# Performance work log

Measured on AMD Instinct MI355X. Metric: run time of the kernel, lower is better.

Reference implementation:

```python
import jax, jax.numpy as jnp
import numpy as np

D_MODEL = 768
N_HEAD = 12
BATCH = 2
SEQ = 2048
MASK_FILL = -100000.0


def setup_inputs() -> dict:
    key = jax.random.key(0)
    ks = jax.random.split(key, 10)
    s = 1.0 / np.sqrt(D_MODEL)
    inp = {
        "xEnc": jax.random.normal(ks[0], (BATCH, SEQ, D_MODEL), jnp.float32),
        "xDec": jax.random.normal(ks[1], (BATCH, SEQ, D_MODEL), jnp.float32),
        # causal mask: True where attention is disallowed (j > i)
        "mask": (jnp.arange(SEQ)[None, :] > jnp.arange(SEQ)[:, None])[None, None, :, :],
        "wQ": jax.random.uniform(ks[2], (D_MODEL, D_MODEL), jnp.float32, -s, s),
        "bQ": jax.random.uniform(ks[3], (D_MODEL,), jnp.float32, -s, s),
        "wK": jax.random.uniform(ks[4], (D_MODEL, D_MODEL), jnp.float32, -s, s),
        "bK": jax.random.uniform(ks[5], (D_MODEL,), jnp.float32, -s, s),
        "wV": jax.random.uniform(ks[6], (D_MODEL, D_MODEL), jnp.float32, -s, s),
        "bV": jax.random.uniform(ks[7], (D_MODEL,), jnp.float32, -s, s),
        "wOut": jax.random.uniform(ks[8], (D_MODEL, D_MODEL), jnp.float32, -s, s),
        "bOut": jax.random.uniform(ks[9], (D_MODEL,), jnp.float32, -s, s),
    }
    return inp


def reference(xEnc, xDec, mask, wQ, bQ, wK, bK, wV, bV, wOut, bOut):
    B, S, D = xEnc.shape
    H = N_HEAD
    Dh = D // H
    # torch Linear: y = x @ W.T + b
    Q = xDec @ wQ.T + bQ
    K = xEnc @ wK.T + bK
    V = xEnc @ wV.T + bV
    Q = Q.reshape(B, S, H, Dh).transpose(0, 2, 1, 3)  # [B,H,S,Dh]
    K = K.reshape(B, S, H, Dh).transpose(0, 2, 1, 3)
    V = V.reshape(B, S, H, Dh).transpose(0, 2, 1, 3)
    score = jnp.einsum("bhqd,bhkd->bhqk", Q, K) / jnp.sqrt(jnp.float32(Dh))
    score = jnp.where(mask, MASK_FILL, score)
    attn = jax.nn.softmax(score, axis=-1)
    ctx = jnp.einsum("bhqk,bhkd->bhqd", attn, V)  # [B,H,S,Dh]
    ctx = ctx.transpose(0, 2, 1, 3).reshape(B, S, D)
    return ctx @ wOut.T + bOut
```

## Files before the change

kernel.cpp:

```cpp
#include <hip/hip_runtime.h>
#include <stdint.h>
#include <stddef.h>

#define DMODEL 768
#define NHEAD 12
#define SEQLEN 2048
#define NBATCH 2
#define DH 64
#define MTOT (NBATCH*SEQLEN)

typedef short s16x4 __attribute__((ext_vector_type(4)));
typedef short s16x8 __attribute__((ext_vector_type(8)));
typedef float f32x4 __attribute__((ext_vector_type(4)));

#define XDECB_OFF 0u
#define XENCB_OFF 3145728u
#define WQB_OFF   6291456u
#define WKB_OFF   6881280u
#define WVB_OFF   7471104u
#define WOUTB_OFF 8060928u
#define QB_OFF    8650752u
#define KB_OFF    11796480u
#define VT_OFF    14942208u
#define CTXB_OFF  18087936u

#define QSCALE 0.18033688011112042f

static __device__ __forceinline__ unsigned short f2bf(float f) {
  union { float f; unsigned int u; } v; v.f = f;
  unsigned int r = v.u + 0x7fffu + ((v.u >> 16) & 1u);
  return (unsigned short)(r >> 16);
}

static __device__ __forceinline__ unsigned int pack2bf(float f0, float f1) {
  union { float f; unsigned int u; } a, b; a.f = f0; b.f = f1;
  return __builtin_amdgcn_perm(b.u + 0x8000u, a.u + 0x8000u, 0x07060302u);
}

#if __has_builtin(__builtin_amdgcn_exp2f)
#define EXP2(x) __builtin_amdgcn_exp2f(x)
#else
#define EXP2(x) exp2f(x)
#endif

static __device__ __forceinline__ f32x4 mfma16(s16x4 a, s16x4 b, f32x4 c) {
  return __builtin_amdgcn_mfma_f32_16x16x16bf16_1k(a, b, c, 0, 0, 0);
}
static __device__ __forceinline__ f32x4 mfma32(s16x8 a, s16x8 b, f32x4 c) {
  return __builtin_amdgcn_mfma_f32_16x16x32_bf16(a, b, c, 0, 0, 0);
}

__global__ __launch_bounds__(256) void cvt_kernel(
    const float* __restrict__ xDec, const float* __restrict__ xEnc,
    const float* __restrict__ wQ, const float* __restrict__ wK,
    const float* __restrict__ wV, const float* __restrict__ wOut,
    unsigned short* __restrict__ ws)
{
  const int seg = blockIdx.y;
  const float* src;
  unsigned int n4, off;
  switch (seg) {
    case 0:  src = xDec; n4 = 786432; off = XDECB_OFF; break;
    case 1:  src = xEnc; n4 = 786432; off = XENCB_OFF; break;
    case 2:  src = wQ;   n4 = 147456; off = WQB_OFF;   break;
    case 3:  src = wK;   n4 = 147456; off = WKB_OFF;   break;
    case 4:  src = wV;   n4 = 147456; off = WVB_OFF;   break;
    default: src = wOut; n4 = 147456; off = WOUTB_OFF; break;
  }
  unsigned short* d = ws + off;
  const unsigned int stride = gridDim.x * blockDim.x;
  for (unsigned int i = blockIdx.x * blockDim.x + threadIdx.x; i < n4; i += stride) {
    const float4 v = ((const float4*)src)[i];
    s16x4 p;
    p[0] = (short)f2bf(v.x); p[1] = (short)f2bf(v.y);
    p[2] = (short)f2bf(v.z); p[3] = (short)f2bf(v.w);
    ((s16x4*)d)[i] = p;
  }
}

#define LSTR 72

__global__ __launch_bounds__(256, 4) void qkv_gemm(
    const unsigned short* __restrict__ xDecB, const unsigned short* __restrict__ xEncB,
    const unsigned short* __restrict__ wQB, const unsigned short* __restrict__ wKB,
    const unsigned short* __restrict__ wVB,
    const float* __restrict__ bQ, const float* __restrict__ bK, const float* __restrict__ bV,
    unsigned short* __restrict__ Qb, unsigned short* __restrict__ Kb,
    unsigned short* __restrict__ Vt)
{
  const int z = blockIdx.z;
  const unsigned short* __restrict__ A = (z == 0) ? xDecB : xEncB;
  const unsigned short* __restrict__ B = (z == 0) ? wQB : ((z == 1) ? wKB : wVB);
  const float* __restrict__ bias = (z == 0) ? bQ : ((z == 1) ? bK : bV);

  __shared__ unsigned short lA[64 * LSTR];
  __shared__ unsigned short lB[128 * LSTR];

  const int tid  = threadIdx.x;
  const int lane = tid & 63;
  const int wid  = tid >> 6;
  const int ln   = lane & 15;
  const int qd   = lane >> 4;
  const int m0 = blockIdx.x * 64;
  const int n0 = blockIdx.y * 128;
  const int wm = (wid & 1) * 32;
  const int wn = (wid >> 1) * 64;

  f32x4 acc[2][4] = {};
  s16x8 pA[2], pB[4];

  auto load_tile = [&](int k0) {
    #pragma unroll
    for (int i = 0; i < 2; ++i) {
      const int f = tid + i * 256;
      pA[i] = *(const s16x8*)(A + (size_t)(m0 + (f >> 3)) * DMODEL + k0 + (f & 7) * 8);
    }
    #pragma unroll
    for (int i = 0; i < 4; ++i) {
      const int f = tid + i * 256;
      pB[i] = *(const s16x8*)(B + (size_t)(n0 + (f >> 3)) * DMODEL + k0 + (f & 7) * 8);
    }
  };

  load_tile(0);
  for (int k0 = 0; k0 < DMODEL; k0 += 64) {
    #pragma unroll
    for (int i = 0; i < 2; ++i) {
      const int f = tid + i * 256;
      *(s16x8*)&lA[(f >> 3) * LSTR + (f & 7) * 8] = pA[i];
    }
    #pragma unroll
    for (int i = 0; i < 4; ++i) {
      const int f = tid + i * 256;
      *(s16x8*)&lB[(f >> 3) * LSTR + (f & 7) * 8] = pB[i];
    }
    __syncthreads();
    if (k0 + 64 < DMODEL) load_tile(k0 + 64);
    #pragma unroll
    for (int kc = 0; kc < 2; ++kc) {
      s16x8 af[2], bfr[4];
      #pragma unroll
      for (int i = 0; i < 2; ++i)
        af[i] = *(const s16x8*)&lA[(wm + i * 16 + ln) * LSTR + kc * 32 + qd * 8];
      #pragma unroll
      for (int j = 0; j < 4; ++j)
        bfr[j] = *(const s16x8*)&lB[(wn + j * 16 + ln) * LSTR + kc * 32 + qd * 8];
      #pragma unroll
      for (int i = 0; i < 2; ++i)
        #pragma unroll
        for (int j = 0; j < 4; ++j)
          acc[i][j] = mfma32(af[i], bfr[j], acc[i][j]);
    }
    __syncthreads();
  }

  #pragma unroll
  for (int j = 0; j < 4; ++j) {
    const int n_g = n0 + wn + j * 16 + ln;
    const float bv = bias[n_g];
    const int h    = n_g >> 6;
    const int dcol = n_g & 63;
    #pragma unroll
    for (int i = 0; i < 2; ++i) {
      #pragma unroll
      for (int r = 0; r < 4; ++r) {
        const int m_g  = m0 + wm + i * 16 + qd * 4 + r;
        const int bb   = m_g >> 11;
        const int srow = m_g & 2047;
        const float val = acc[i][j][r] + bv;
        if (z == 0)
          Qb[((size_t)((bb * NHEAD + h) * SEQLEN + srow)) * DH + dcol] = f2bf(val * QSCALE);
        else if (z == 1)
          Kb[((size_t)((bb * NHEAD + h) * SEQLEN + srow)) * DH + dcol] = f2bf(val);
        else
          Vt[((size_t)((bb * NHEAD + h) * DH + dcol)) * SEQLEN + srow] = f2bf(val);
      }
    }
  }
}

__global__ __launch_bounds__(256, 4) void out_gemm(
    const unsigned short* __restrict__ ctx, const unsigned short* __restrict__ wOutB,
    const float* __restrict__ bOut, float* __restrict__ out)
{
  __shared__ unsigned short lA[64 * LSTR];
  __shared__ unsigned short lB[128 * LSTR];

  const int tid  = threadIdx.x;
  const int lane = tid & 63;
  const int wid  = tid >> 6;
  const int ln   = lane & 15;
  const int qd   = lane >> 4;
  const int m0 = blockIdx.x * 64;
  const int n0 = blockIdx.y * 128;
  const int wm = (wid & 1) * 32;
  const int wn = (wid >> 1) * 64;

  f32x4 acc[2][4] = {};
  s16x8 pA[2], pB[4];

  auto load_tile = [&](int k0) {
    #pragma unroll
    for (int i = 0; i < 2; ++i) {
      const int f = tid + i * 256;
      pA[i] = *(const s16x8*)(ctx + (size_t)(m0 + (f >> 3)) * DMODEL + k0 + (f & 7) * 8);
    }
    #pragma unroll
    for (int i = 0; i < 4; ++i) {
      const int f = tid + i * 256;
      pB[i] = *(const s16x8*)(wOutB + (size_t)(n0 + (f >> 3)) * DMODEL + k0 + (f & 7) * 8);
    }
  };

  load_tile(0);
  for (int k0 = 0; k0 < DMODEL; k0 += 64) {
    #pragma unroll
    for (int i = 0; i < 2; ++i) {
      const int f = tid + i * 256;
      *(s16x8*)&lA[(f >> 3) * LSTR + (f & 7) * 8] = pA[i];
    }
    #pragma unroll
    for (int i = 0; i < 4; ++i) {
      const int f = tid + i * 256;
      *(s16x8*)&lB[(f >> 3) * LSTR + (f & 7) * 8] = pB[i];
    }
    __syncthreads();
    if (k0 + 64 < DMODEL) load_tile(k0 + 64);
    #pragma unroll
    for (int kc = 0; kc < 2; ++kc) {
      s16x8 af[2], bfr[4];
      #pragma unroll
      for (int i = 0; i < 2; ++i)
        af[i] = *(const s16x8*)&lA[(wm + i * 16 + ln) * LSTR + kc * 32 + qd * 8];
      #pragma unroll
      for (int j = 0; j < 4; ++j)
        bfr[j] = *(const s16x8*)&lB[(wn + j * 16 + ln) * LSTR + kc * 32 + qd * 8];
      #pragma unroll
      for (int i = 0; i < 2; ++i)
        #pragma unroll
        for (int j = 0; j < 4; ++j)
          acc[i][j] = mfma32(af[i], bfr[j], acc[i][j]);
    }
    __syncthreads();
  }

  #pragma unroll
  for (int j = 0; j < 4; ++j) {
    const int n_g = n0 + wn + j * 16 + ln;
    const float bv = bOut[n_g];
    #pragma unroll
    for (int i = 0; i < 2; ++i) {
      #pragma unroll
      for (int r = 0; r < 4; ++r) {
        const int m_g = m0 + wm + i * 16 + qd * 4 + r;
        out[(size_t)m_g * DMODEL + n_g] = acc[i][j][r] + bv;
      }
    }
  }
}

#define KVT 128
#define LKP 72
#define LVP 136

__global__ __launch_bounds__(256, 3) void attn_kernel(
    const unsigned short* __restrict__ Qb, const unsigned short* __restrict__ Kb,
    const unsigned short* __restrict__ Vt, unsigned short* __restrict__ ctx)
{
  __shared__ unsigned short lK[KVT * LKP];
  __shared__ unsigned short lV[DH * LVP];

  const int tid  = threadIdx.x;
  const int lane = tid & 63;
  const int wid  = tid >> 6;
  const int ln   = lane & 15;
  const int qd   = lane >> 4;
  const int bh = blockIdx.y;
  const int q0 = (gridDim.x - 1 - blockIdx.x) * 64;
  const int q_lane = q0 + wid * 16 + ln;

  s16x8 qf[2];
  {
    const unsigned short* Qrow = Qb + ((size_t)bh * SEQLEN + q_lane) * DH;
    qf[0] = *(const s16x8*)(Qrow + qd * 8);
    qf[1] = *(const s16x8*)(Qrow + 32 + qd * 8);
  }

  float m_run = -__builtin_inff();
  float l_run = 0.0f;
  f32x4 o_acc[4] = {};

  const unsigned short* Kbase = Kb + (size_t)bh * SEQLEN * DH;
  const unsigned short* Vbase = Vt + (size_t)bh * DH * SEQLEN;
  const int kv_end = q0 + 64;
  const int ntiles = (kv_end + KVT - 1) / KVT;

  s16x8 rK[4], rV[4];
  auto load_kv = [&](int kv0) {
    #pragma unroll
    for (int i = 0; i < 4; ++i) {
      const int f = tid + i * 256;
      rK[i] = *(const s16x8*)(Kbase + (size_t)(kv0 + (f >> 3)) * DH + (f & 7) * 8);
    }
    #pragma unroll
    for (int i = 0; i < 4; ++i) {
      const int f = tid + i * 256;
      rV[i] = *(const s16x8*)(Vbase + (size_t)(f >> 4) * SEQLEN + kv0 + (f & 15) * 8);
    }
  };

  load_kv(0);
  for (int t0 = 0; t0 < ntiles; ++t0) {
    const int kv0 = t0 * KVT;
    #pragma unroll
    for (int i = 0; i < 4; ++i) {
      const int f = tid + i * 256;
      *(s16x8*)&lK[(f >> 3) * LKP + (f & 7) * 8] = rK[i];
    }
    #pragma unroll
    for (int i = 0; i < 4; ++i) {
      const int f = tid + i * 256;
      *(s16x8*)&lV[(f >> 4) * LVP + (f & 15) * 8] = rV[i];
    }
    __syncthreads();
    if (t0 + 1 < ntiles) load_kv(kv0 + KVT);

    f32x4 s_acc[8] = {};
    #pragma unroll
    for (int kc = 0; kc < 2; ++kc) {
      #pragma unroll
      for (int t = 0; t < 8; ++t) {
        const s16x8 a = *(const s16x8*)&lK[(t * 16 + ln) * LKP + kc * 32 + qd * 8];
        s_acc[t] = mfma32(a, qf[kc], s_acc[t]);
      }
    }

    float tmax = -1e30f;
    if (kv0 + KVT > q0) {
      #pragma unroll
      for (int t = 0; t < 8; ++t) {
        #pragma unroll
        for (int r = 0; r < 4; ++r) {
          const int kv = kv0 + t * 16 + qd * 4 + r;
          float sv = s_acc[t][r];
          sv = (kv > q_lane) ? -1e30f : sv;
          s_acc[t][r] = sv;
          tmax = fmaxf(tmax, sv);
        }
      }
    } else {
      #pragma unroll
      for (int t = 0; t < 8; ++t) {
        #pragma unroll
        for (int r = 0; r < 4; ++r)
          tmax = fmaxf(tmax, s_acc[t][r]);
      }
    }
    tmax = fmaxf(tmax, __shfl_xor(tmax, 16));
    tmax = fmaxf(tmax, __shfl_xor(tmax, 32));
    const float m_new = fmaxf(m_run, tmax);
    const float alpha = EXP2(m_run - m_new);

    float rsum = 0.0f;
    s16x4 pf[8];
    #pragma unroll
    for (int t = 0; t < 8; ++t) {
      const float p0 = EXP2(s_acc[t][0] - m_new);
      const float p1 = EXP2(s_acc[t][1] - m_new);
      const float p2 = EXP2(s_acc[t][2] - m_new);
      const float p3 = EXP2(s_acc[t][3] - m_new);
      rsum += (p0 + p1) + (p2 + p3);
      union { unsigned int u[2]; s16x4 v; } pk;
      pk.u[0] = pack2bf(p0, p1);
      pk.u[1] = pack2bf(p2, p3);
      pf[t] = pk.v;
    }
    rsum += __shfl_xor(rsum, 16);
    rsum += __shfl_xor(rsum, 32);
    l_run = l_run * alpha + rsum;
    m_run = m_new;

    #pragma unroll
    for (int r = 0; r < 4; ++r) {
      const float ar = __shfl(alpha, qd * 4 + r);
      #pragma unroll
      for (int j = 0; j < 4; ++j) o_acc[j][r] *= ar;
    }

    #pragma unroll
    for (int t = 0; t < 8; ++t) {
      #pragma unroll
      for (int j = 0; j < 4; ++j) {
        const s16x4 b = *(const s16x4*)&lV[(j * 16 + ln) * LVP + t * 16 + qd * 4];
        o_acc[j] = mfma16(pf[t], b, o_acc[j]);
      }
    }
    __syncthreads();
  }

  const int bb = bh / NHEAD;
  const int h  = bh % NHEAD;
  #pragma unroll
  for (int r = 0; r < 4; ++r) {
    const float lr  = __shfl(l_run, qd * 4 + r);
    const float inv = 1.0f / lr;
    const int q_g = q0 + wid * 16 + qd * 4 + r;
    unsigned short* dst = ctx + ((size_t)bb * SEQLEN + q_g) * DMODEL + h * DH;
    #pragma unroll
    for (int j = 0; j < 4; ++j)
      dst[j * 16 + ln] = f2bf(o_acc[j][r] * inv);
  }
}

extern "C" void kernel_launch(void* const* d_in, const int* in_sizes, int n_in,
                              void* d_out, int out_size, void* d_ws, size_t ws_size,
                              hipStream_t stream)
{
  const float* xEnc = (const float*)d_in[0];
  const float* xDec = (const float*)d_in[1];
  const float* wQ   = (const float*)d_in[3];
  const float* bQ   = (const float*)d_in[4];
  const float* wK   = (const float*)d_in[5];
  const float* bK   = (const float*)d_in[6];
  const float* wV   = (const float*)d_in[7];
  const float* bV   = (const float*)d_in[8];
  const float* wOut = (const float*)d_in[9];
  const float* bOut = (const float*)d_in[10];

  unsigned short* ws = (unsigned short*)d_ws;

  cvt_kernel<<<dim3(512, 6), 256, 0, stream>>>(xDec, xEnc, wQ, wK, wV, wOut, ws);
  qkv_gemm<<<dim3(MTOT / 64, DMODEL / 128, 3), 256, 0, stream>>>(
      ws + XDECB_OFF, ws + XENCB_OFF, ws + WQB_OFF, ws + WKB_OFF, ws + WVB_OFF,
      bQ, bK, bV, ws + QB_OFF, ws + KB_OFF, ws + VT_OFF);
  attn_kernel<<<dim3(SEQLEN / 64, NBATCH * NHEAD), 256, 0, stream>>>(
      ws + QB_OFF, ws + KB_OFF, ws + VT_OFF, ws + CTXB_OFF);
  out_gemm<<<dim3(MTOT / 64, DMODEL / 128), 256, 0, stream>>>(
      ws + CTXB_OFF, ws + WOUTB_OFF, bOut, (float*)d_out);
}
```

Measured before the change: 201.5 us.

## Drop LDS staging in attention; load K/V fragments directly from global per wave

The attention kernel no longer stages K and V tiles through shared memory with block-wide barriers. Each wave now reads its K fragments straight from global memory into registers, prefetching the next 64-row tile, and reads V fragments directly from global inside the PV MFMA loop. The KV tile shrinks from 128 to 64, and each wave gets its own causal tile count, so waves no longer sync and skip tiles past their own diagonal. The cost is redundant global/L2 traffic, since all four waves read the same K/V, and V loads are exposed with no prefetch.

```diff
diff --git a/kernel.cpp b/kernel.cpp
--- a/kernel.cpp
+++ b/kernel.cpp
@@ -259,25 +259,18 @@
   }
 }
 
-#define KVT 128
-#define LKP 72
-#define LVP 136
-
 __global__ __launch_bounds__(256, 3) void attn_kernel(
     const unsigned short* __restrict__ Qb, const unsigned short* __restrict__ Kb,
     const unsigned short* __restrict__ Vt, unsigned short* __restrict__ ctx)
 {
-  __shared__ unsigned short lK[KVT * LKP];
-  __shared__ unsigned short lV[DH * LVP];
-
   const int tid  = threadIdx.x;
   const int lane = tid & 63;
   const int wid  = tid >> 6;
   const int ln   = lane & 15;
   const int qd   = lane >> 4;
   const int bh = blockIdx.y;
-  const int q0 = (gridDim.x - 1 - blockIdx.x) * 64;
-  const int q_lane = q0 + wid * 16 + ln;
+  const int qb = (gridDim.x - 1 - blockIdx.x) * 64 + wid * 16;
+  const int q_lane = qb + ln;
 
   s16x8 qf[2];
   {
@@ -292,53 +285,40 @@
 
   const unsigned short* Kbase = Kb + (size_t)bh * SEQLEN * DH;
   const unsigned short* Vbase = Vt + (size_t)bh * DH * SEQLEN;
-  const int kv_end = q0 + 64;
-  const int ntiles = (kv_end + KVT - 1) / KVT;
-
-  s16x8 rK[4], rV[4];
-  auto load_kv = [&](int kv0) {
-    #pragma unroll
-    for (int i = 0; i < 4; ++i) {
-      const int f = tid + i * 256;
-      rK[i] = *(const s16x8*)(Kbase + (size_t)(kv0 + (f >> 3)) * DH + (f & 7) * 8);
-    }
-    #pragma unroll
-    for (int i = 0; i < 4; ++i) {
-      const int f = tid + i * 256;
-      rV[i] = *(const s16x8*)(Vbase + (size_t)(f >> 4) * SEQLEN + kv0 + (f & 15) * 8);
-    }
-  };
-
-  load_kv(0);
+  const int ntiles = (qb + 79) >> 6;
+
+  s16x8 rK[4][2], rKn[4][2];
+  #pragma unroll
+  for (int t = 0; t < 4; ++t) {
+    const unsigned short* Krow = Kbase + (size_t)(t * 16 + ln) * DH + qd * 8;
+    rK[t][0] = *(const s16x8*)(Krow);
+    rK[t][1] = *(const s16x8*)(Krow + 32);
+  }
+
   for (int t0 = 0; t0 < ntiles; ++t0) {
-    const int kv0 = t0 * KVT;
-    #pragma unroll
-    for (int i = 0; i < 4; ++i) {
-      const int f = tid + i * 256;
-      *(s16x8*)&lK[(f >> 3) * LKP + (f & 7) * 8] = rK[i];
-    }
-    #pragma unroll
-    for (int i = 0; i < 4; ++i) {
-      const int f = tid + i * 256;
-      *(s16x8*)&lV[(f >> 4) * LVP + (f & 15) * 8] = rV[i];
-    }
-    __syncthreads();
-    if (t0 + 1 < ntiles) load_kv(kv0 + KVT);
-
-    f32x4 s_acc[8] = {};
-    #pragma unroll
-    for (int kc = 0; kc < 2; ++kc) {
-      #pragma unroll
-      for (int t = 0; t < 8; ++t) {
-        const s16x8 a = *(const s16x8*)&lK[(t * 16 + ln) * LKP + kc * 32 + qd * 8];
-        s_acc[t] = mfma32(a, qf[kc], s_acc[t]);
+    const int kv0 = t0 * 64;
+
+    f32x4 s_acc[4] = {};
+    #pragma unroll
+    for (int t = 0; t < 4; ++t) {
+      s_acc[t] = mfma32(rK[t][0], qf[0], s_acc[t]);
+      s_acc[t] = mfma32(rK[t][1], qf[1], s_acc[t]);
+    }
+
+    if (t0 + 1 < ntiles) {
+      #pragma unroll
+      for (int t = 0; t < 4; ++t) {
+        const unsigned short* Krow =
+            Kbase + (size_t)(kv0 + 64 + t * 16 + ln) * DH + qd * 8;
+        rKn[t][0] = *(const s16x8*)(Krow);
+        rKn[t][1] = *(const s16x8*)(Krow + 32);
       }
     }
 
     float tmax = -1e30f;
-    if (kv0 + KVT > q0) {
-      #pragma unroll
-      for (int t = 0; t < 8; ++t) {
+    if (kv0 + 64 > qb) {
+      #pragma unroll
+      for (int t = 0; t < 4; ++t) {
         #pragma unroll
         for (int r = 0; r < 4; ++r) {
           const int kv = kv0 + t * 16 + qd * 4 + r;
@@ -350,7 +330,7 @@
       }
     } else {
       #pragma unroll
-      for (int t = 0; t < 8; ++t) {
+      for (int t = 0; t < 4; ++t) {
         #pragma unroll
         for (int r = 0; r < 4; ++r)
           tmax = fmaxf(tmax, s_acc[t][r]);
@@ -362,9 +342,9 @@
     const float alpha = EXP2(m_run - m_new);
 
     float rsum = 0.0f;
-    s16x4 pf[8];
-    #pragma unroll
-    for (int t = 0; t < 8; ++t) {
+    s16x4 pf[4];
+    #pragma unroll
+    for (int t = 0; t < 4; ++t) {
       const float p0 = EXP2(s_acc[t][0] - m_new);
       const float p1 = EXP2(s_acc[t][1] - m_new);
       const float p2 = EXP2(s_acc[t][2] - m_new);
@@ -388,14 +368,20 @@
     }
 
     #pragma unroll
-    for (int t = 0; t < 8; ++t) {
+    for (int t = 0; t < 4; ++t) {
       #pragma unroll
       for (int j = 0; j < 4; ++j) {
-        const s16x4 b = *(const s16x4*)&lV[(j * 16 + ln) * LVP + t * 16 + qd * 4];
+        const s16x4 b = *(const s16x4*)(
+            Vbase + (size_t)(j * 16 + ln) * SEQLEN + kv0 + t * 16 + qd * 4);
         o_acc[j] = mfma16(pf[t], b, o_acc[j]);
       }
     }
-    __syncthreads();
+
+    #pragma unroll
+    for (int t = 0; t < 4; ++t) {
+      rK[t][0] = rKn[t][0];
+      rK[t][1] = rKn[t][1];
+    }
   }
 
   const int bb = bh / NHEAD;
@@ -404,7 +390,7 @@
   for (int r = 0; r < 4; ++r) {
     const float lr  = __shfl(l_run, qd * 4 + r);
     const float inv = 1.0f / lr;
-    const int q_g = q0 + wid * 16 + qd * 4 + r;
+    const int q_g = qb + qd * 4 + r;
     unsigned short* dst = ctx + ((size_t)bb * SEQLEN + q_g) * DMODEL + h * DH;
     #pragma unroll
     for (int j = 0; j < 4; ++j)
```

New measurement: 401.5 us. +99.2%, slower.
